# Kernel tuning notes

Measured on AMD Instinct MI355X. Metric: run time of the kernel, lower is better.

Reference implementation:

```python
import jax, jax.numpy as jnp
import numpy as np

B, S, D = 2, 1024, 4096
N_HEADS, KV_HEADS, HEAD_DIM = 32, 8, 128
EPS = 1e-6
ROPE_THETA = 1e6


def setup_inputs() -> dict:
    key = jax.random.key(0)
    ks = jax.random.split(key, 7)
    scale = 0.02
    x = jax.random.normal(ks[0], (B, S, D), dtype=jnp.float32)
    positions = jnp.broadcast_to(jnp.arange(S, dtype=jnp.int32)[None, :], (B, S))
    wq = jax.random.normal(ks[1], (D, N_HEADS, HEAD_DIM), dtype=jnp.float32) * scale
    wk = jax.random.normal(ks[2], (D, KV_HEADS, HEAD_DIM), dtype=jnp.float32) * scale
    wv = jax.random.normal(ks[3], (D, KV_HEADS, HEAD_DIM), dtype=jnp.float32) * scale
    wo = jax.random.normal(ks[4], (N_HEADS, HEAD_DIM, D), dtype=jnp.float32) * scale
    q_norm_w = 1.0 + jax.random.normal(ks[5], (HEAD_DIM,), dtype=jnp.float32) * 0.01
    k_norm_w = 1.0 + jax.random.normal(ks[6], (HEAD_DIM,), dtype=jnp.float32) * 0.01
    return {"x": x, "positions": positions, "wq": wq, "wk": wk, "wv": wv,
            "wo": wo, "q_norm_w": q_norm_w, "k_norm_w": k_norm_w}


def _rms_norm(t, w):
    # per-head RMSNorm over last (head_dim) axis
    var = jnp.mean(jnp.square(t), axis=-1, keepdims=True)
    return (t * jax.lax.rsqrt(var + EPS)) * w


def _rope(t, positions):
    # neox-style rotary embedding; t: [B, S, n, H], positions: [B, S]
    half = t.shape[-1] // 2
    inv_freq = 1.0 / (ROPE_THETA ** (jnp.arange(0, half, dtype=jnp.float32) / half))
    ang = positions.astype(jnp.float32)[..., None] * inv_freq  # [B, S, half]
    cos = jnp.cos(ang)[:, :, None, :]  # [B, S, 1, half]
    sin = jnp.sin(ang)[:, :, None, :]
    t1, t2 = t[..., :half], t[..., half:]
    return jnp.concatenate([t1 * cos - t2 * sin, t2 * cos + t1 * sin], axis=-1)


def reference(x, positions, wq, wk, wv, wo, q_norm_w, k_norm_w):
    # QKV projections (einsum layers: 'bsd,dnh->bsnh')
    q = jnp.einsum('bsd,dnh->bsnh', x, wq)  # [B, S, N, H]
    k = jnp.einsum('bsd,dkh->bskh', x, wk)  # [B, S, K, H]
    v = jnp.einsum('bsd,dkh->bskh', x, wv)
    # per-head QK RMSNorm, then RoPE
    q = _rope(_rms_norm(q, q_norm_w), positions)
    k = _rope(_rms_norm(k, k_norm_w), positions)
    # GQA: expand KV heads to query heads
    groups = N_HEADS // KV_HEADS
    k = jnp.repeat(k, groups, axis=2)  # [B, S, N, H]
    v = jnp.repeat(v, groups, axis=2)
    sm_scale = HEAD_DIM ** -0.5
    scores = jnp.einsum('bqnh,btnh->bnqt', q, k) * sm_scale  # [B, N, S, S]
    causal = jnp.tril(jnp.ones((S, S), dtype=bool))
    scores = jnp.where(causal[None, None], scores, jnp.finfo(scores.dtype).min)
    probs = jax.nn.softmax(scores, axis=-1)
    attn = jnp.einsum('bnqt,btnh->bqnh', probs, v)  # [B, S, N, H]
    out = jnp.einsum('bqnh,nhd->bqd', attn, wo)  # output projection
    return out
```

## Files before the change

kernel.cpp:

```cpp
#include <hip/hip_runtime.h>
#include <stdint.h>

#define S_LEN   1024
#define D_MODEL 4096
#define NHQ     32
#define NKV     8
#define HD      128
#define NTOK    2048
#define NQKV    6144
#define SM_SCALE 0.08838834764831843f

typedef __attribute__((ext_vector_type(8))) __bf16 bf16x8;
typedef __attribute__((ext_vector_type(4))) float f32x4;

__device__ __forceinline__ unsigned short f2bf(float f) {
  union { float f; unsigned u; } x; x.f = f;
  unsigned r = x.u + 0x7fffu + ((x.u >> 16) & 1u);
  return (unsigned short)(r >> 16);
}

__device__ __forceinline__ void gload_lds16(const void* g, void* l) {
  __builtin_amdgcn_global_load_lds((__attribute__((address_space(1))) void*)g,
                                   (__attribute__((address_space(3))) void*)l,
                                   16, 0, 0);
}

__global__ void k_f32_to_bf16(const float* __restrict__ in,
                              unsigned short* __restrict__ out, int n8) {
  int i = blockIdx.x * blockDim.x + threadIdx.x;
  if (i >= n8) return;
  const float4* p = (const float4*)(in + (size_t)i * 8);
  float4 v0 = p[0], v1 = p[1];
  uint4 o;
  o.x = f2bf(v0.x) | ((unsigned)f2bf(v0.y) << 16);
  o.y = f2bf(v0.z) | ((unsigned)f2bf(v0.w) << 16);
  o.z = f2bf(v1.x) | ((unsigned)f2bf(v1.y) << 16);
  o.w = f2bf(v1.z) | ((unsigned)f2bf(v1.w) << 16);
  *(uint4*)(out + (size_t)i * 8) = o;
}

__global__ void k_transpose(const float* __restrict__ in,
                            unsigned short* __restrict__ out, int R, int C) {
  __shared__ float t[32][33];
  int c = threadIdx.x & 31, r0 = threadIdx.x >> 5;
  int cb = blockIdx.x * 32, rb = blockIdx.y * 32;
#pragma unroll
  for (int i = 0; i < 4; ++i) {
    int r = r0 + i * 8;
    t[r][c] = in[(size_t)(rb + r) * C + cb + c];
  }
  __syncthreads();
#pragma unroll
  for (int i = 0; i < 4; ++i) {
    int r = r0 + i * 8;
    out[(size_t)(cb + r) * R + rb + c] = f2bf(t[c][r]);
  }
}


#define STG(Gptr, rowbase, ksrc, half, bufi, matoff)                            \
  { int kcl = (ksrc) < NT ? (ksrc) : NT - 1;                                    \
    _Pragma("unroll")                                                           \
    for (int i_ = 0; i_ < 2; ++i_) {                                            \
      int lin = i_ * 512 + tid;                                                 \
      int r_ = lin >> 2, slot = lin & 3;                                        \
      int sw = slot ^ ((r_ >> 1) & 3);                                          \
      gload_lds16(Gptr + (size_t)((rowbase) + r_) * Kstride + k0e + kcl * 64 + (half) * 32 + sw * 8, \
                  smem + (bufi) * 65536 + (matoff) + (half) * 16384 + lin * 16); \
    } }

#define RD_A(mh, kh, bufi)                                                      \
  _Pragma("unroll")                                                             \
  for (int mf = 0; mf < 4; ++mf) {                                              \
    int row = wr * 128 + (mh) * 64 + mf * 16 + lr;                              \
    af[mf] = *(const bf16x8*)(smem + (bufi) * 65536 + (kh) * 16384 + row * 64   \
                              + ((lg * 16) ^ (((row >> 1) & 3) << 4)));         \
  }

#define RD_B(kh, bufi)                                                          \
  _Pragma("unroll")                                                             \
  for (int nf = 0; nf < 4; ++nf) {                                              \
    int row = wc * 64 + nf * 16 + lr;                                           \
    bf[nf] = *(const bf16x8*)(smem + (bufi) * 65536 + 32768 + (kh) * 16384 + row * 64 \
                              + ((lg * 16) ^ (((row >> 1) & 3) << 4)));         \
  }

#define PHASE_TAIL(mh, GATE)                                                    \
  if (GATE) asm volatile("s_waitcnt vmcnt(4)" ::: "memory");                    \
  __builtin_amdgcn_s_barrier();                                                 \
  asm volatile("s_waitcnt lgkmcnt(0)" ::: "memory");                            \
  __builtin_amdgcn_sched_barrier(0);                                            \
  __builtin_amdgcn_s_setprio(1);                                                \
  _Pragma("unroll")                                                             \
  for (int mf = 0; mf < 4; ++mf)                                                \
    _Pragma("unroll")                                                           \
    for (int nf = 0; nf < 4; ++nf)                                              \
      acc[(mh) * 4 + mf][nf] = __builtin_amdgcn_mfma_f32_16x16x32_bf16(         \
          af[mf], bf[nf], acc[(mh) * 4 + mf][nf], 0, 0, 0);                     \
  __builtin_amdgcn_s_setprio(0);                                                \
  __builtin_amdgcn_s_barrier();

__global__ __launch_bounds__(512, 2) void k_gemm256(
    const unsigned short* __restrict__ A,
    const unsigned short* __restrict__ Bt,
    float* __restrict__ C, int Kstride, int ldc, int nbx, int ksplit, int NT,
    int use_atomic) {
  extern __shared__ __align__(16) char smem[];
  int tid = threadIdx.x;
  int l = tid & 63;
  int w = tid >> 6;
  int lr = l & 15, lg = l >> 4;
  int wr = w >> 2, wc = w & 3;
  int nwg = gridDim.x;
  int q8 = nwg >> 3;
  int o = blockIdx.x;
  int wg = (o & 7) * q8 + (o >> 3);
  int tiles = nwg / ksplit;
  int ks = wg / tiles;
  int wgt = wg - ks * tiles;
  int by = wgt / nbx, bx = wgt - by * nbx;
  int bm = by * 256, bn = bx * 256;
  int k0e = ks * NT * 64;

  f32x4 acc[8][4] = {};
  bf16x8 af[4], bf[4];

  STG(A, bm, 0, 0, 0, 0); STG(Bt, bn, 0, 0, 0, 32768);
  STG(A, bm, 0, 1, 0, 0); STG(Bt, bn, 0, 1, 0, 32768);
  asm volatile("s_waitcnt vmcnt(4)" ::: "memory");
  __builtin_amdgcn_s_barrier();

  for (int kt = 0; kt < NT; ++kt) {
    int cur = kt & 1;
    RD_A(0, 0, cur) RD_B(0, cur)
    STG(A, bm, kt + 1, 0, cur ^ 1, 0)
    PHASE_TAIL(0, 0)
    RD_A(1, 0, cur)
    STG(Bt, bn, kt + 1, 0, cur ^ 1, 32768)
    PHASE_TAIL(1, 1)
    RD_A(0, 1, cur) RD_B(1, cur)
    STG(A, bm, kt + 1, 1, cur ^ 1, 0)
    PHASE_TAIL(0, 0)
    RD_A(1, 1, cur)
    STG(Bt, bn, kt + 1, 1, cur ^ 1, 32768)
    PHASE_TAIL(1, 1)
  }

#pragma unroll
  for (int mh = 0; mh < 2; ++mh)
#pragma unroll
    for (int mf = 0; mf < 4; ++mf)
#pragma unroll
      for (int nf = 0; nf < 4; ++nf)
#pragma unroll
        for (int j = 0; j < 4; ++j) {
          size_t idx = (size_t)(bm + wr * 128 + mh * 64 + mf * 16 + lg * 4 + j) * ldc +
                       bn + wc * 64 + nf * 16 + lr;
          float v = acc[mh * 4 + mf][nf][j];
          if (use_atomic) atomicAdd(&C[idx], v);
          else C[idx] = v;
        }
}

__global__ void k_norm_rope(const float* __restrict__ qkv, const float* __restrict__ w,
                            const int* __restrict__ positions,
                            unsigned short* __restrict__ out, int nheads, int colbase,
                            float oscale) {
  int wid = blockIdx.x * 4 + (threadIdx.x >> 6);
  int lane = threadIdx.x & 63;
  int token = wid / nheads, head = wid - token * nheads;
  const float* src = qkv + (size_t)token * NQKV + colbase + head * HD;
  float e0 = src[lane], e1 = src[lane + 64];
  float ss = e0 * e0 + e1 * e1;
#pragma unroll
  for (int m = 1; m < 64; m <<= 1) ss += __shfl_xor(ss, m, 64);
  float rs = rsqrtf(ss * (1.0f / 128.0f) + 1e-6f);
  float n0 = e0 * rs * w[lane], n1 = e1 * rs * w[lane + 64];
  int pos = positions[token];
  float invf = exp2f((float)lane * (-19.931568569324174f / 64.0f));
  float ang = (float)pos * invf;
  float sv, cv;
  sincosf(ang, &sv, &cv);
  float o0 = (n0 * cv - n1 * sv) * oscale;
  float o1 = (n1 * cv + n0 * sv) * oscale;
  int b = token >> 10, s = token & 1023;
  size_t ob = ((size_t)(b * nheads + head) * S_LEN + s) * HD;
  out[ob + lane] = f2bf(o0);
  out[ob + 64 + lane] = f2bf(o1);
}

__global__ void k_v_transpose(const float* __restrict__ qkv, unsigned short* __restrict__ vt) {
  __shared__ float t[32][33];
  int slice = blockIdx.z;
  int b = slice >> 3, kh = slice & 7;
  const float* in = qkv + (size_t)(b * S_LEN) * NQKV + 5120 + kh * HD;
  unsigned short* out = vt + (size_t)slice * HD * S_LEN;
  int c = threadIdx.x & 31, r0 = threadIdx.x >> 5;
  int s0 = blockIdx.y * 32, d0 = blockIdx.x * 32;
#pragma unroll
  for (int i = 0; i < 4; ++i) {
    int r = r0 + i * 8;
    t[r][c] = in[(size_t)(s0 + r) * NQKV + d0 + c];
  }
  __syncthreads();
#pragma unroll
  for (int i = 0; i < 4; ++i) {
    int r = r0 + i * 8;
    out[(size_t)(d0 + r) * S_LEN + s0 + c] = f2bf(t[c][r]);
  }
}

__global__ __launch_bounds__(256) void k_attn(const unsigned short* __restrict__ qh,
                                              const unsigned short* __restrict__ kbuf,
                                              const unsigned short* __restrict__ vtbuf,
                                              unsigned short* __restrict__ attn_out) {
  __shared__ __align__(16) unsigned short k_lds[64 * 128];
  __shared__ __align__(16) unsigned short v_lds[128 * 64];
  __shared__ __align__(16) unsigned short p_lds[4][16 * 64];
  int b = blockIdx.z, h = blockIdx.y, bx = blockIdx.x;
  int khd = h >> 2;
  int tid = threadIdx.x, w = tid >> 6, l = tid & 63;
  int lr = l & 15, lg = l >> 4;
  const unsigned short* K = kbuf + (size_t)(b * NKV + khd) * S_LEN * HD;
  const unsigned short* VT = vtbuf + (size_t)(b * NKV + khd) * HD * S_LEN;
  char* klp = (char*)k_lds;
  char* vlp = (char*)v_lds;
  char* plp = (char*)p_lds[w];
  int swz = (lr & 7) << 4;

  for (int strip = 0; strip < 2; ++strip) {
    int qs = strip ? (15 - bx) : bx;
    int q0 = qs * 64;
    const unsigned short* Q = qh + ((size_t)(b * NHQ + h) * S_LEN + q0 + w * 16) * HD;
    bf16x8 qf[4];
#pragma unroll
    for (int kk = 0; kk < 4; ++kk)
      qf[kk] = *(const bf16x8*)&Q[(size_t)lr * HD + kk * 32 + lg * 8];

    f32x4 o[8] = {};
    float m_[4], l_[4];
#pragma unroll
    for (int j = 0; j < 4; ++j) { m_[j] = -1e30f; l_[j] = 0.0f; }

    int nt = qs + 1;
    for (int t = 0; t < nt; ++t) {
      int t0 = t * 64;
      __syncthreads();
#pragma unroll
      for (int it = 0; it < 4; ++it) {
        int db = (tid + it * 256) * 16;
        int kr = db >> 8, kc = db & 255;
        gload_lds16(K + (size_t)(t0 + kr) * HD + ((kc ^ ((kr & 7) << 4)) >> 1), klp + db);
        int vr = db >> 7, vc = db & 127;
        gload_lds16(VT + (size_t)vr * S_LEN + t0 + ((vc ^ ((vr & 7) << 4)) >> 1), vlp + db);
      }
      __syncthreads();

      f32x4 sc[4];
      __builtin_amdgcn_s_setprio(1);
#pragma unroll
      for (int ct = 0; ct < 4; ++ct) {
        f32x4 s = {};
        int row = ct * 16 + lr;
#pragma unroll
        for (int kk = 0; kk < 4; ++kk) {
          bf16x8 kf = *(const bf16x8*)(klp + row * 256 + ((kk * 64 + lg * 16) ^ swz));
          s = __builtin_amdgcn_mfma_f32_16x16x32_bf16(qf[kk], kf, s, 0, 0, 0);
        }
        sc[ct] = s;
      }
      __builtin_amdgcn_s_setprio(0);

      bool full = (t < qs);
      float alpha[4];
#pragma unroll
      for (int j = 0; j < 4; ++j) {
        if (!full) {
          int rg = q0 + w * 16 + lg * 4 + j;
#pragma unroll
          for (int ct = 0; ct < 4; ++ct)
            sc[ct][j] = (t0 + ct * 16 + lr <= rg) ? sc[ct][j] : -1e30f;
        }
        float mx = fmaxf(fmaxf(sc[0][j], sc[1][j]), fmaxf(sc[2][j], sc[3][j]));
#pragma unroll
        for (int msk = 1; msk < 16; msk <<= 1) mx = fmaxf(mx, __shfl_xor(mx, msk, 64));
        float mn = fmaxf(m_[j], mx);
        alpha[j] = __expf(m_[j] - mn);
        int q = lg * 4 + j;
        int psw = (q & 7) << 4;
        float ps = 0.0f;
#pragma unroll
        for (int ct = 0; ct < 4; ++ct) {
          float p = __expf(sc[ct][j] - mn);
          ps += p;
          *(unsigned short*)(plp + q * 128 + (((ct * 16 + lr) * 2) ^ psw)) = f2bf(p);
        }
#pragma unroll
        for (int msk = 1; msk < 16; msk <<= 1) ps += __shfl_xor(ps, msk, 64);
        l_[j] = l_[j] * alpha[j] + ps;
        m_[j] = mn;
      }
#pragma unroll
      for (int dc = 0; dc < 8; ++dc) {
        o[dc][0] *= alpha[0]; o[dc][1] *= alpha[1];
        o[dc][2] *= alpha[2]; o[dc][3] *= alpha[3];
      }
      asm volatile("s_waitcnt lgkmcnt(0)" ::: "memory");
      __builtin_amdgcn_s_setprio(1);
#pragma unroll
      for (int kt = 0; kt < 2; ++kt) {
        bf16x8 pa = *(const bf16x8*)(plp + lr * 128 + ((kt * 64 + lg * 16) ^ swz));
#pragma unroll
        for (int dc = 0; dc < 8; ++dc) {
          int vrow = dc * 16 + lr;
          bf16x8 vf = *(const bf16x8*)(vlp + vrow * 128 + ((kt * 64 + lg * 16) ^ swz));
          o[dc] = __builtin_amdgcn_mfma_f32_16x16x32_bf16(pa, vf, o[dc], 0, 0, 0);
        }
      }
      __builtin_amdgcn_s_setprio(0);
    }

#pragma unroll
    for (int j = 0; j < 4; ++j) {
      int rg = q0 + w * 16 + lg * 4 + j;
      size_t row = (size_t)(b * S_LEN + rg) * D_MODEL + h * HD;
      float inv = 1.0f / l_[j];
#pragma unroll
      for (int dc = 0; dc < 8; ++dc)
        attn_out[row + dc * 16 + lr] = f2bf(o[dc][j] * inv);
    }
  }
}

extern "C" void kernel_launch(void* const* d_in, const int* in_sizes, int n_in,
                              void* d_out, int out_size, void* d_ws, size_t ws_size,
                              hipStream_t stream) {
  const float* x        = (const float*)d_in[0];
  const int* positions  = (const int*)d_in[1];
  const float* wq       = (const float*)d_in[2];
  const float* wk       = (const float*)d_in[3];
  const float* wv       = (const float*)d_in[4];
  const float* wo       = (const float*)d_in[5];
  const float* qnw      = (const float*)d_in[6];
  const float* knw      = (const float*)d_in[7];
  float* out            = (float*)d_out;

  char* ws = (char*)d_ws;
  unsigned short* xb   = (unsigned short*)(ws);
  unsigned short* wB   = (unsigned short*)(ws + 16777216);
  unsigned short* woT  = (unsigned short*)(ws + 67108864);
  float*          qkv  = (float*)(ws + 100663296);
  unsigned short* qh   = wB;
  unsigned short* khb  = (unsigned short*)(ws + 33554432);
  unsigned short* vtb  = (unsigned short*)(ws + 37748736);
  unsigned short* attn = xb;

  dim3 tb(256);
  hipMemsetAsync(out, 0, (size_t)out_size * 4, stream);

  k_f32_to_bf16<<<4096, tb, 0, stream>>>(x, xb, 1048576);
  k_transpose<<<dim3(128, 128), tb, 0, stream>>>(wq, wB, 4096, 4096);
  k_transpose<<<dim3(32, 128), tb, 0, stream>>>(wk, wB + (size_t)4096 * 4096, 4096, 1024);
  k_transpose<<<dim3(32, 128), tb, 0, stream>>>(wv, wB + (size_t)5120 * 4096, 4096, 1024);
  k_transpose<<<dim3(128, 128), tb, 0, stream>>>(wo, woT, 4096, 4096);

  k_gemm256<<<dim3(192), dim3(512), 131072, stream>>>(xb, wB, qkv, 4096, 6144, 24, 1, 64, 0);

  k_norm_rope<<<16384, tb, 0, stream>>>(qkv, qnw, positions, qh, 32, 0, SM_SCALE);
  k_norm_rope<<<4096, tb, 0, stream>>>(qkv, knw, positions, khb, 8, 4096, 1.0f);
  k_v_transpose<<<dim3(4, 32, 16), tb, 0, stream>>>(qkv, vtb);

  k_attn<<<dim3(8, 32, 2), tb, 0, stream>>>(qh, khb, vtb, attn);

  k_gemm256<<<dim3(256), dim3(512), 131072, stream>>>(attn, woT, out, 4096, 4096, 16, 2, 32, 1);
}
```

Before: 375.4 us.

## Template GEMM on N-tile width, drop split-K atomics, emit bf16 QKV

The GEMM is templated on N-fragment count. The output projection now uses 256x128 tiles over the full K range, with plain stores in place of split-K atomicAdd, so the output memset is removed. The QKV projection writes bf16 instead of fp32, which halves intermediate traffic, and the norm/rope and V-transpose kernels now read bf16. Tile-to-XCD mapping is reorganized into grouped blocks per XCD. The bf16 QKV intermediate rounds values before RMSNorm, costing some precision.

Result: faster. 324.2 us (-13.7%).

```diff
diff --git a/kernel.cpp b/kernel.cpp
--- a/kernel.cpp
+++ b/kernel.cpp
@@ -17,6 +17,9 @@
   union { float f; unsigned u; } x; x.f = f;
   unsigned r = x.u + 0x7fffu + ((x.u >> 16) & 1u);
   return (unsigned short)(r >> 16);
+}
+__device__ __forceinline__ float bf2f(unsigned short u) {
+  union { unsigned u; float f; } x; x.u = (unsigned)u << 16; return x.f;
 }
 
 __device__ __forceinline__ void gload_lds16(const void* g, void* l) {
@@ -58,35 +61,50 @@
 }
 
 
-#define STG(Gptr, rowbase, ksrc, half, bufi, matoff)                            \
+#define STGA(ksrc, half, bufi)                                                  \
   { int kcl = (ksrc) < NT ? (ksrc) : NT - 1;                                    \
     _Pragma("unroll")                                                           \
     for (int i_ = 0; i_ < 2; ++i_) {                                            \
       int lin = i_ * 512 + tid;                                                 \
       int r_ = lin >> 2, slot = lin & 3;                                        \
       int sw = slot ^ ((r_ >> 1) & 3);                                          \
-      gload_lds16(Gptr + (size_t)((rowbase) + r_) * Kstride + k0e + kcl * 64 + (half) * 32 + sw * 8, \
-                  smem + (bufi) * 65536 + (matoff) + (half) * 16384 + lin * 16); \
+      gload_lds16(Aptr + (size_t)(bm + r_) * Kstride + kcl * 64 + (half) * 32 + sw * 8, \
+                  smem + (bufi) * BUFST + (half) * 16384 + lin * 16);           \
+    } }
+
+#define STGB(ksrc, half, bufi)                                                  \
+  { int kcl = (ksrc) < NT ? (ksrc) : NT - 1;                                    \
+    _Pragma("unroll")                                                           \
+    for (int i_ = 0; i_ < NF / 2; ++i_) {                                       \
+      int lin = i_ * 512 + tid;                                                 \
+      int r_ = lin >> 2, slot = lin & 3;                                        \
+      int sw = slot ^ ((r_ >> 1) & 3);                                          \
+      gload_lds16(Bptr + (size_t)(bn + r_) * Kstride + kcl * 64 + (half) * 32 + sw * 8, \
+                  smem + (bufi) * BUFST + 32768 + (half) * (NF * 4096) + lin * 16); \
     } }
 
 #define RD_A(mh, kh, bufi)                                                      \
   _Pragma("unroll")                                                             \
   for (int mf = 0; mf < 4; ++mf) {                                              \
     int row = wr * 128 + (mh) * 64 + mf * 16 + lr;                              \
-    af[mf] = *(const bf16x8*)(smem + (bufi) * 65536 + (kh) * 16384 + row * 64   \
+    af[mf] = *(const bf16x8*)(smem + (bufi) * BUFST + (kh) * 16384 + row * 64   \
                               + ((lg * 16) ^ (((row >> 1) & 3) << 4)));         \
   }
 
 #define RD_B(kh, bufi)                                                          \
   _Pragma("unroll")                                                             \
-  for (int nf = 0; nf < 4; ++nf) {                                              \
-    int row = wc * 64 + nf * 16 + lr;                                           \
-    bf[nf] = *(const bf16x8*)(smem + (bufi) * 65536 + 32768 + (kh) * 16384 + row * 64 \
-                              + ((lg * 16) ^ (((row >> 1) & 3) << 4)));         \
-  }
+  for (int nf = 0; nf < NF; ++nf) {                                             \
+    int row = wc * NF * 16 + nf * 16 + lr;                                      \
+    bf[nf] = *(const bf16x8*)(smem + (bufi) * BUFST + 32768 + (kh) * (NF * 4096) \
+                              + row * 64 + ((lg * 16) ^ (((row >> 1) & 3) << 4))); \
+  }
+
+#define GATEW                                                                   \
+  { if constexpr (NF == 4) asm volatile("s_waitcnt vmcnt(4)" ::: "memory");     \
+    else                   asm volatile("s_waitcnt vmcnt(3)" ::: "memory"); }
 
 #define PHASE_TAIL(mh, GATE)                                                    \
-  if (GATE) asm volatile("s_waitcnt vmcnt(4)" ::: "memory");                    \
+  if (GATE) GATEW                                                               \
   __builtin_amdgcn_s_barrier();                                                 \
   asm volatile("s_waitcnt lgkmcnt(0)" ::: "memory");                            \
   __builtin_amdgcn_sched_barrier(0);                                            \
@@ -94,55 +112,53 @@
   _Pragma("unroll")                                                             \
   for (int mf = 0; mf < 4; ++mf)                                                \
     _Pragma("unroll")                                                           \
-    for (int nf = 0; nf < 4; ++nf)                                              \
+    for (int nf = 0; nf < NF; ++nf)                                             \
       acc[(mh) * 4 + mf][nf] = __builtin_amdgcn_mfma_f32_16x16x32_bf16(         \
           af[mf], bf[nf], acc[(mh) * 4 + mf][nf], 0, 0, 0);                     \
   __builtin_amdgcn_s_setprio(0);                                                \
   __builtin_amdgcn_s_barrier();
 
-__global__ __launch_bounds__(512, 2) void k_gemm256(
-    const unsigned short* __restrict__ A,
-    const unsigned short* __restrict__ Bt,
-    float* __restrict__ C, int Kstride, int ldc, int nbx, int ksplit, int NT,
-    int use_atomic) {
+template <int NF, typename OutT>
+__global__ __launch_bounds__(512, 1) void k_gemm256(
+    const unsigned short* __restrict__ Aptr,
+    const unsigned short* __restrict__ Bptr,
+    OutT* __restrict__ C, int Kstride, int ldc, int NT, int SGN, int nxn) {
   extern __shared__ __align__(16) char smem[];
+  constexpr int BUFST = 32768 + NF * 8192;
   int tid = threadIdx.x;
   int l = tid & 63;
   int w = tid >> 6;
   int lr = l & 15, lg = l >> 4;
   int wr = w >> 2, wc = w & 3;
-  int nwg = gridDim.x;
-  int q8 = nwg >> 3;
-  int o = blockIdx.x;
-  int wg = (o & 7) * q8 + (o >> 3);
-  int tiles = nwg / ksplit;
-  int ks = wg / tiles;
-  int wgt = wg - ks * tiles;
-  int by = wgt / nbx, bx = wgt - by * nbx;
-  int bm = by * 256, bn = bx * 256;
-  int k0e = ks * NT * 64;
-
-  f32x4 acc[8][4] = {};
-  bf16x8 af[4], bf[4];
-
-  STG(A, bm, 0, 0, 0, 0); STG(Bt, bn, 0, 0, 0, 32768);
-  STG(A, bm, 0, 1, 0, 0); STG(Bt, bn, 0, 1, 0, 32768);
-  asm volatile("s_waitcnt vmcnt(4)" ::: "memory");
+  int per_xcd = gridDim.x >> 3;
+  int x8 = blockIdx.x & 7, i = blockIdx.x >> 3;
+  int SGM = per_xcd / SGN;
+  int xr = x8 / nxn, xc = x8 - xr * nxn;
+  int iy = i / SGN;
+  int by = xr * SGM + iy, bx = xc * SGN + (i - iy * SGN);
+  int bm = by * 256, bn = bx * NF * 64;
+
+  f32x4 acc[8][NF] = {};
+  bf16x8 af[4], bf[NF];
+
+  STGA(0, 0, 0) STGB(0, 0, 0)
+  STGA(0, 1, 0) STGB(0, 1, 0)
+  GATEW
   __builtin_amdgcn_s_barrier();
 
   for (int kt = 0; kt < NT; ++kt) {
     int cur = kt & 1;
     RD_A(0, 0, cur) RD_B(0, cur)
-    STG(A, bm, kt + 1, 0, cur ^ 1, 0)
+    STGA(kt + 1, 0, cur ^ 1)
     PHASE_TAIL(0, 0)
     RD_A(1, 0, cur)
-    STG(Bt, bn, kt + 1, 0, cur ^ 1, 32768)
+    STGB(kt + 1, 0, cur ^ 1)
     PHASE_TAIL(1, 1)
     RD_A(0, 1, cur) RD_B(1, cur)
-    STG(A, bm, kt + 1, 1, cur ^ 1, 0)
+    STGA(kt + 1, 1, cur ^ 1)
     PHASE_TAIL(0, 0)
     RD_A(1, 1, cur)
-    STG(Bt, bn, kt + 1, 1, cur ^ 1, 32768)
+    STGB(kt + 1, 1, cur ^ 1)
     PHASE_TAIL(1, 1)
   }
 
@@ -151,26 +167,27 @@
 #pragma unroll
     for (int mf = 0; mf < 4; ++mf)
 #pragma unroll
-      for (int nf = 0; nf < 4; ++nf)
+      for (int nf = 0; nf < NF; ++nf)
 #pragma unroll
         for (int j = 0; j < 4; ++j) {
           size_t idx = (size_t)(bm + wr * 128 + mh * 64 + mf * 16 + lg * 4 + j) * ldc +
-                       bn + wc * 64 + nf * 16 + lr;
+                       bn + wc * NF * 16 + nf * 16 + lr;
           float v = acc[mh * 4 + mf][nf][j];
-          if (use_atomic) atomicAdd(&C[idx], v);
+          if constexpr (sizeof(OutT) == 2) C[idx] = f2bf(v);
           else C[idx] = v;
         }
 }
 
-__global__ void k_norm_rope(const float* __restrict__ qkv, const float* __restrict__ w,
+__global__ void k_norm_rope(const unsigned short* __restrict__ qkv,
+                            const float* __restrict__ w,
                             const int* __restrict__ positions,
                             unsigned short* __restrict__ out, int nheads, int colbase,
                             float oscale) {
   int wid = blockIdx.x * 4 + (threadIdx.x >> 6);
   int lane = threadIdx.x & 63;
   int token = wid / nheads, head = wid - token * nheads;
-  const float* src = qkv + (size_t)token * NQKV + colbase + head * HD;
-  float e0 = src[lane], e1 = src[lane + 64];
+  const unsigned short* src = qkv + (size_t)token * NQKV + colbase + head * HD;
+  float e0 = bf2f(src[lane]), e1 = bf2f(src[lane + 64]);
   float ss = e0 * e0 + e1 * e1;
 #pragma unroll
   for (int m = 1; m < 64; m <<= 1) ss += __shfl_xor(ss, m, 64);
@@ -189,11 +206,12 @@
   out[ob + 64 + lane] = f2bf(o1);
 }
 
-__global__ void k_v_transpose(const float* __restrict__ qkv, unsigned short* __restrict__ vt) {
-  __shared__ float t[32][33];
+__global__ void k_v_transpose(const unsigned short* __restrict__ qkv,
+                              unsigned short* __restrict__ vt) {
+  __shared__ unsigned short t[32][33];
   int slice = blockIdx.z;
   int b = slice >> 3, kh = slice & 7;
-  const float* in = qkv + (size_t)(b * S_LEN) * NQKV + 5120 + kh * HD;
+  const unsigned short* in = qkv + (size_t)(b * S_LEN) * NQKV + 5120 + kh * HD;
   unsigned short* out = vt + (size_t)slice * HD * S_LEN;
   int c = threadIdx.x & 31, r0 = threadIdx.x >> 5;
   int s0 = blockIdx.y * 32, d0 = blockIdx.x * 32;
@@ -206,7 +224,7 @@
 #pragma unroll
   for (int i = 0; i < 4; ++i) {
     int r = r0 + i * 8;
-    out[(size_t)(d0 + r) * S_LEN + s0 + c] = f2bf(t[c][r]);
+    out[(size_t)(d0 + r) * S_LEN + s0 + c] = t[c][r];
   }
 }
 
@@ -349,28 +367,28 @@
   unsigned short* xb   = (unsigned short*)(ws);
   unsigned short* wB   = (unsigned short*)(ws + 16777216);
   unsigned short* woT  = (unsigned short*)(ws + 67108864);
-  float*          qkv  = (float*)(ws + 100663296);
+  unsigned short* qkvb = (unsigned short*)(ws + 100663296);
   unsigned short* qh   = wB;
   unsigned short* khb  = (unsigned short*)(ws + 33554432);
   unsigned short* vtb  = (unsigned short*)(ws + 37748736);
   unsigned short* attn = xb;
 
   dim3 tb(256);
-  hipMemsetAsync(out, 0, (size_t)out_size * 4, stream);
-
   k_f32_to_bf16<<<4096, tb, 0, stream>>>(x, xb, 1048576);
   k_transpose<<<dim3(128, 128), tb, 0, stream>>>(wq, wB, 4096, 4096);
   k_transpose<<<dim3(32, 128), tb, 0, stream>>>(wk, wB + (size_t)4096 * 4096, 4096, 1024);
   k_transpose<<<dim3(32, 128), tb, 0, stream>>>(wv, wB + (size_t)5120 * 4096, 4096, 1024);
   k_transpose<<<dim3(128, 128), tb, 0, stream>>>(wo, woT, 4096, 4096);
 
-  k_gemm256<<<dim3(192), dim3(512), 131072, stream>>>(xb, wB, qkv, 4096, 6144, 24, 1, 64, 0);
-
-  k_norm_rope<<<16384, tb, 0, stream>>>(qkv, qnw, positions, qh, 32, 0, SM_SCALE);
-  k_norm_rope<<<4096, tb, 0, stream>>>(qkv, knw, positions, khb, 8, 4096, 1.0f);
-  k_v_transpose<<<dim3(4, 32, 16), tb, 0, stream>>>(qkv, vtb);
+  k_gemm256<4, unsigned short><<<dim3(192), dim3(512), 131072, stream>>>(
+      xb, wB, qkvb, 4096, 6144, 64, 6, 4);
+
+  k_norm_rope<<<16384, tb, 0, stream>>>(qkvb, qnw, positions, qh, 32, 0, SM_SCALE);
+  k_norm_rope<<<4096, tb, 0, stream>>>(qkvb, knw, positions, khb, 8, 4096, 1.0f);
+  k_v_transpose<<<dim3(4, 32, 16), tb, 0, stream>>>(qkvb, vtb);
 
   k_attn<<<dim3(8, 32, 2), tb, 0, stream>>>(qh, khb, vtb, attn);
 
-  k_gemm256<<<dim3(256), dim3(512), 131072, stream>>>(attn, woT, out, 4096, 4096, 16, 2, 32, 1);
-}
+  k_gemm256<2, float><<<dim3(256), dim3(512), 98304, stream>>>(
+      attn, woT, out, 4096, 4096, 64, 8, 4);
+}
```
